# Optimization experiments

Measured on AMD Instinct MI355X. Metric: run time of the kernel, lower is better.

The kernel has to match this reference:

```python
import jax, jax.numpy as jnp
import numpy as np

B, T, D, H = 32, 256, 1024, 1024


def _flip_sequences(x, lengths):
    # Flip only the valid (unpadded) prefix of each sequence, as in flax sst2 util.
    max_len = x.shape[1]
    idxs = (jnp.arange(max_len - 1, -1, -1)[None, :] + lengths[:, None]) % max_len
    return x[jnp.arange(x.shape[0])[:, None], idxs]


def _lstm(x, Wi, Wh, b):
    # OptimizedLSTMCell math: z = x@Wi + h@Wh + b; gates (i, f, g, o);
    # c' = sig(f)*c + sig(i)*tanh(g); h' = sig(o)*tanh(c')
    batch = x.shape[0]
    hid = Wh.shape[0]
    xg = jnp.einsum('btd,dk->btk', x, Wi) + b  # precompute input projections [B,T,4H]

    def step(carry, xg_t):
        c, h = carry
        z = xg_t + h @ Wh
        i, f, g, o = jnp.split(z, 4, axis=-1)
        c = jax.nn.sigmoid(f) * c + jax.nn.sigmoid(i) * jnp.tanh(g)
        h = jax.nn.sigmoid(o) * jnp.tanh(c)
        return (c, h), h

    init = (jnp.zeros((batch, hid), x.dtype), jnp.zeros((batch, hid), x.dtype))
    _, hs = jax.lax.scan(step, init, jnp.swapaxes(xg, 0, 1))  # scan over time
    return jnp.swapaxes(hs, 0, 1)  # [B,T,H]


def setup_inputs() -> dict:
    key = jax.random.key(0)
    ks = jax.random.split(key, 7)
    si = 1.0 / np.sqrt(D)
    sh = 1.0 / np.sqrt(H)
    x = jax.random.normal(ks[0], (B, T, D), dtype=jnp.float32)
    mask = jnp.ones((B, T), dtype=jnp.int32)
    Wi_f = jax.random.normal(ks[1], (D, 4 * H), jnp.float32) * si
    Wh_f = jax.random.normal(ks[2], (H, 4 * H), jnp.float32) * sh
    b_f = jnp.zeros((4 * H,), jnp.float32)
    Wi_b = jax.random.normal(ks[3], (D, 4 * H), jnp.float32) * si
    Wh_b = jax.random.normal(ks[4], (H, 4 * H), jnp.float32) * sh
    b_b = jnp.zeros((4 * H,), jnp.float32)
    return {"x": x, "mask": mask, "Wi_f": Wi_f, "Wh_f": Wh_f, "b_f": b_f,
            "Wi_b": Wi_b, "Wh_b": Wh_b, "b_b": b_b}


def reference(x, mask, Wi_f, Wh_f, b_f, Wi_b, Wh_b, b_b):
    lengths = jnp.sum(mask, axis=1)
    fwd = _lstm(x, Wi_f, Wh_f, b_f)
    x_rev = _flip_sequences(x, lengths)
    bwd = _lstm(x_rev, Wi_b, Wh_b, b_b)
    bwd = _flip_sequences(bwd, lengths)
    return jnp.concatenate([fwd, bwd], axis=-1)  # [B,T,2H]
```

## Files before the change

### kernel.cpp

```cpp
#include <hip/hip_runtime.h>
#include <hip/hip_bf16.h>
#include <stdint.h>

typedef __attribute__((ext_vector_type(4))) float f32x4;
typedef __attribute__((ext_vector_type(8))) short short8;
typedef __attribute__((ext_vector_type(4))) short short4v;

#define OFF_XBF  ((size_t)0)
#define OFF_WIT  ((size_t)16777216)
#define OFF_WHT  ((size_t)33554432)
#define OFF_XG   ((size_t)50331648)
#define OFF_H    ((size_t)184549376)
#define OFF_BIAS ((size_t)184811520)
#define OFF_LEN  ((size_t)184844288)
#define OFF_CNT  ((size_t)184844416)

__device__ __forceinline__ short f2bf(float f) {
  union { float f; uint32_t u; } v; v.f = f;
  uint32_t u = v.u;
  uint32_t r = (u + 0x7fffu + ((u >> 16) & 1u)) >> 16;
  return (short)r;
}
__device__ __forceinline__ float bf2f(short s) {
  union { uint32_t u; float f; } v; v.u = ((uint32_t)(uint16_t)s) << 16;
  return v.f;
}
__device__ __forceinline__ float sigf(float z) {
  float e = __builtin_amdgcn_exp2f(z * -1.44269504f);
  return __builtin_amdgcn_rcpf(1.f + e);
}
__device__ __forceinline__ float tanhfast(float z) {
  float e = __builtin_amdgcn_exp2f(z * -2.88539008f);
  return fmaf(__builtin_amdgcn_rcpf(1.f + e), 2.f, -1.f);
}

__global__ void k_len(const int* __restrict__ mask, int* __restrict__ len) {
  int b = threadIdx.x;
  if (b < 32) {
    int s = 0;
    for (int t = 0; t < 256; t++) s += mask[b * 256 + t];
    len[b] = s;
  }
}

__global__ void k_xconv(const float* __restrict__ x, short* __restrict__ xbf) {
  int bid = blockIdx.x;
  int b = bid >> 8, t = bid & 255;
  int d = threadIdx.x * 4;
  const float* sp = x + ((size_t)bid) * 1024 + d;
  float4 v = *(const float4*)sp;
  short4v o;
  o.x = f2bf(v.x); o.y = f2bf(v.y); o.z = f2bf(v.z); o.w = f2bf(v.w);
  *(short4v*)(xbf + ((size_t)(t * 32 + b)) * 1024 + d) = o;
}

__global__ void k_wprep(const float* __restrict__ Wi_f, const float* __restrict__ Wi_b,
                        const float* __restrict__ Wh_f, const float* __restrict__ Wh_b,
                        short* __restrict__ WiT, short* __restrict__ WhT) {
  __shared__ short ldsT[64 * 72];
  int id = blockIdx.x;
  int which = id >> 11, dir = (id >> 10) & 1, tile = id & 1023;
  int kt = (tile >> 6) * 64, c0 = (tile & 63) * 64;
  const float* src = (which == 0) ? (dir == 0 ? Wi_f : Wi_b)
                                  : (dir == 0 ? Wh_f : Wh_b);
  short* dst = (which == 0) ? WiT : WhT;
  int tid = threadIdx.x;
#pragma unroll 4
  for (int i = 0; i < 16; i++) {
    int idx = i * 256 + tid;
    int kk = idx >> 6, cc = idx & 63;
    float v = src[(size_t)(kt + kk) * 4096 + c0 + cc];
    ldsT[cc * 72 + kk] = f2bf(v);
  }
  __syncthreads();
  int rowc = tid >> 2, part = tid & 3;
  int cg = c0 + rowc;
  int gate = cg >> 10, hc = cg & 1023;
  int p = (hc >> 2) * 16 + gate * 4 + (hc & 3);
  int n = dir * 4096 + p;
  short8 v0 = *(short8*)&ldsT[rowc * 72 + part * 16];
  short8 v1 = *(short8*)&ldsT[rowc * 72 + part * 16 + 8];
  *(short8*)(dst + (size_t)n * 1024 + kt + part * 16) = v0;
  *(short8*)(dst + (size_t)n * 1024 + kt + part * 16 + 8) = v1;
}

__global__ void k_bias(const float* __restrict__ bf_, const float* __restrict__ bb_,
                       float* __restrict__ bp) {
  int n = blockIdx.x * 256 + threadIdx.x;
  int dir = n >> 12, p = n & 4095;
  int gate = (p >> 2) & 3, g4 = p >> 4, h4 = p & 3;
  int c = gate * 1024 + g4 * 4 + h4;
  bp[n] = (dir == 0 ? bf_ : bb_)[c];
}

__global__ void k_gemm(const short* __restrict__ Abf,
                       const short* __restrict__ Bbf,
                       const float* __restrict__ bias,
                       short* __restrict__ C) {
  __shared__ char Ash[128 * 144];
  __shared__ char Bsh[128 * 144];
  const int tid = threadIdx.x;
  const int lane = tid & 63, wid = tid >> 6;
  const int wm = wid >> 1, wn = wid & 1;
  const int l15 = lane & 15, lg = lane >> 4;
  const int m0 = blockIdx.y * 128, n0 = blockIdx.x * 128;

  f32x4 acc[4][4];
#pragma unroll
  for (int i = 0; i < 4; i++)
#pragma unroll
    for (int j = 0; j < 4; j++) acc[i][j] = (f32x4){0.f, 0.f, 0.f, 0.f};

  for (int kt = 0; kt < 1024; kt += 64) {
#pragma unroll
    for (int i = 0; i < 4; i++) {
      int chunk = i * 256 + tid;
      int row = chunk >> 3, kc = chunk & 7;
      *(short8*)(Ash + row * 144 + kc * 16) =
          *(const short8*)(Abf + (size_t)(m0 + row) * 1024 + kt + kc * 8);
      *(short8*)(Bsh + row * 144 + kc * 16) =
          *(const short8*)(Bbf + (size_t)(n0 + row) * 1024 + kt + kc * 8);
    }
    __syncthreads();
#pragma unroll
    for (int kk = 0; kk < 2; kk++) {
      short8 af[4], bfv[4];
#pragma unroll
      for (int mt = 0; mt < 4; mt++)
        af[mt] = *(const short8*)(Ash + (wm * 64 + mt * 16 + l15) * 144 + kk * 64 + lg * 16);
#pragma unroll
      for (int ntc = 0; ntc < 4; ntc++)
        bfv[ntc] = *(const short8*)(Bsh + (wn * 64 + ntc * 16 + l15) * 144 + kk * 64 + lg * 16);
#pragma unroll
      for (int mt = 0; mt < 4; mt++)
#pragma unroll
        for (int ntc = 0; ntc < 4; ntc++)
          acc[mt][ntc] = __builtin_amdgcn_mfma_f32_16x16x32_bf16(af[mt], bfv[ntc], acc[mt][ntc], 0, 0, 0);
    }
    __syncthreads();
  }
  float bs[4];
#pragma unroll
  for (int ntc = 0; ntc < 4; ntc++) bs[ntc] = bias[n0 + wn * 64 + ntc * 16 + l15];
#pragma unroll
  for (int mt = 0; mt < 4; mt++) {
    int row = m0 + wm * 64 + mt * 16 + lg * 4;
#pragma unroll
    for (int ntc = 0; ntc < 4; ntc++) {
      int col = n0 + wn * 64 + ntc * 16 + l15;
#pragma unroll
      for (int r = 0; r < 4; r++)
        C[(size_t)(row + r) * 8192 + col] = f2bf(acc[mt][ntc][r] + bs[ntc]);
    }
  }
}

__global__ void __launch_bounds__(512, 1) k_recur(
    const short* __restrict__ XG,
    const short* __restrict__ WhT,
    const int* __restrict__ len,
    short* __restrict__ hbuf,
    float* __restrict__ out,
    unsigned int* __restrict__ flags) {
  __shared__ char Hld[65536];
  const int tid = threadIdx.x;
  const int lane = tid & 63;
  const int wid = tid >> 6;
  const int bidx = blockIdx.x;
  const int dir = bidx >> 6;
  const int nblk = bidx & 63;
  const int mt = wid >> 2, nt = wid & 3;
  const int l15 = lane & 15, lg = lane >> 4;

  const int ncol = dir * 4096 + nblk * 64 + nt * 16 + l15;
  const short* wrow = WhT + (size_t)ncol * 1024;
  short8 bfr[32];
#pragma unroll
  for (int kk = 0; kk < 32; kk++)
    bfr[kk] = *(const short8*)(wrow + kk * 32 + lg * 8);

  float c_reg[4] = {0.f, 0.f, 0.f, 0.f};
  int lenv[4];
#pragma unroll
  for (int r = 0; r < 4; r++) lenv[r] = len[mt * 16 + lg * 4 + r];

  const int c4 = l15;
  const int gate = c4 >> 2;
  const int brow = mt * 16 + l15;
  const int sw = (brow & 7) << 4;
  const int abase = brow * 2048 + (lg << 4);
  const int hcol0 = nblk * 16 + nt * 4;
  unsigned int* dflags = flags + dir * 64;

  float xg_pf[4];
#pragma unroll
  for (int r = 0; r < 4; r++) {
    int b_r = mt * 16 + lg * 4 + r;
    int tt = (dir == 0) ? 0 : ((lenv[r] - 1) & 255);
    xg_pf[r] = bf2f(XG[(size_t)(tt * 32 + b_r) * 8192 + ncol]);
  }

  for (int t = 0; t < 256; t++) {
    const short* hsrc = hbuf + (size_t)(((t & 1) * 2 + dir) * 32768);
    {
      f32x4 sv[8];
#pragma unroll
      for (int i = 0; i < 8; i++) {
        const short* a = hsrc + (i * 512 + tid) * 8;
        asm volatile("global_load_dwordx4 %0, %1, off sc0 sc1"
                     : "=v"(sv[i]) : "v"(a));
      }
      asm volatile("s_waitcnt vmcnt(0)" ::: "memory");
      __builtin_amdgcn_sched_barrier(0);
#pragma unroll
      for (int i = 0; i < 8; i++) {
        int chunk = i * 512 + tid;
        int row = chunk >> 7;
        *(f32x4*)(Hld + ((chunk * 16) ^ ((row & 7) << 4))) = sv[i];
      }
    }
    __syncthreads();

    f32x4 accA = (f32x4){0.f, 0.f, 0.f, 0.f};
    f32x4 accB = (f32x4){0.f, 0.f, 0.f, 0.f};
#pragma unroll
    for (int kk = 0; kk < 16; kk++) {
      short8 afA = *(const short8*)(Hld + ((abase + kk * 64) ^ sw));
      short8 afB = *(const short8*)(Hld + ((abase + (kk + 16) * 64) ^ sw));
      accA = __builtin_amdgcn_mfma_f32_16x16x32_bf16(afA, bfr[kk], accA, 0, 0, 0);
      accB = __builtin_amdgcn_mfma_f32_16x16x32_bf16(afB, bfr[kk + 16], accB, 0, 0, 0);
    }

    f32x4 hsave[4];
#pragma unroll
    for (int r = 0; r < 4; r++) {
      int b_r = mt * 16 + lg * 4 + r;
      float z = accA[r] + accB[r] + xg_pf[r];
      float s = (gate == 2) ? tanhfast(z) : sigf(z);
      float x8 = __shfl_xor(s, 8);
      float pI = s * x8;
      float v = (gate == 0) ? pI : s;
      float x4 = __shfl_xor(v, 4);
      float o4 = __shfl_xor(x8, 4);
      float cn = fmaf(x4, c_reg[r], pI);
      float h = o4 * tanhfast(cn);
      if (c4 < 4) c_reg[r] = cn;
      uint32_t hb = (uint32_t)(uint16_t)f2bf(h);
      uint32_t p0 = hb | (__shfl_xor(hb, 1) << 16);
      uint32_t q  = __shfl_xor(p0, 2);
      if (c4 == 0) {
        unsigned long long p = (unsigned long long)p0 | ((unsigned long long)q << 32);
        unsigned long long* haddr = (unsigned long long*)
          (hbuf + (size_t)((((t + 1) & 1) * 2 + dir) * 32768) + b_r * 1024 + hcol0);
        __hip_atomic_store(haddr, p, __ATOMIC_RELAXED, __HIP_MEMORY_SCOPE_AGENT);
        hsave[r].x = bf2f((short)(p0 & 0xffff));
        hsave[r].y = bf2f((short)(p0 >> 16));
        hsave[r].z = bf2f((short)(q & 0xffff));
        hsave[r].w = bf2f((short)(q >> 16));
      }
    }

    asm volatile("s_waitcnt vmcnt(0)" ::: "memory");
    __syncthreads();
    if (tid == 0) {
      __hip_atomic_store(dflags + nblk, (unsigned int)(t + 1),
                         __ATOMIC_RELAXED, __HIP_MEMORY_SCOPE_AGENT);
    }
    __builtin_amdgcn_sched_barrier(0);

    if (c4 == 0) {
#pragma unroll
      for (int r = 0; r < 4; r++) {
        int b_r = mt * 16 + lg * 4 + r;
        int tt = (dir == 0) ? t : ((lenv[r] - 1 - t) & 255);
        *(f32x4*)(out + ((size_t)b_r * 256 + tt) * 2048 + dir * 1024 + hcol0) = hsave[r];
      }
    }
    int tn = (t < 255) ? t + 1 : 255;
#pragma unroll
    for (int r = 0; r < 4; r++) {
      int b_r = mt * 16 + lg * 4 + r;
      int tt = (dir == 0) ? tn : ((lenv[r] - 1 - tn) & 255);
      xg_pf[r] = bf2f(XG[(size_t)(tt * 32 + b_r) * 8192 + ncol]);
    }

    if (wid == 0) {
      const unsigned int* fl = dflags + lane;
      unsigned int tgt = (unsigned int)(t + 1);
      for (;;) {
        unsigned int v = __hip_atomic_load(fl, __ATOMIC_RELAXED, __HIP_MEMORY_SCOPE_AGENT);
        if (__all((int)(v >= tgt))) break;
      }
    }
    __builtin_amdgcn_sched_barrier(0);
    __syncthreads();
  }
}

extern "C" void kernel_launch(void* const* d_in, const int* in_sizes, int n_in,
                              void* d_out, int out_size, void* d_ws, size_t ws_size,
                              hipStream_t stream) {
  const float* x    = (const float*)d_in[0];
  const int*   mask = (const int*)d_in[1];
  const float* Wi_f = (const float*)d_in[2];
  const float* Wh_f = (const float*)d_in[3];
  const float* b_f  = (const float*)d_in[4];
  const float* Wi_b = (const float*)d_in[5];
  const float* Wh_b = (const float*)d_in[6];
  const float* b_b  = (const float*)d_in[7];
  float* out = (float*)d_out;
  char* ws = (char*)d_ws;

  short* xbf  = (short*)(ws + OFF_XBF);
  short* WiT  = (short*)(ws + OFF_WIT);
  short* WhT  = (short*)(ws + OFF_WHT);
  short* XG   = (short*)(ws + OFF_XG);
  short* hbuf = (short*)(ws + OFF_H);
  float* bp   = (float*)(ws + OFF_BIAS);
  int*   len  = (int*)(ws + OFF_LEN);
  unsigned int* flags = (unsigned int*)(ws + OFF_CNT);

  hipMemsetAsync(hbuf, 0, 262144, stream);
  hipMemsetAsync(flags, 0, 512, stream);

  k_len<<<1, 64, 0, stream>>>(mask, len);
  k_xconv<<<8192, 256, 0, stream>>>(x, xbf);
  k_wprep<<<4096, 256, 0, stream>>>(Wi_f, Wi_b, Wh_f, Wh_b, WiT, WhT);
  k_bias<<<32, 256, 0, stream>>>(b_f, b_b, bp);

  dim3 g(64, 64);
  k_gemm<<<g, 256, 0, stream>>>(xbf, WiT, bp, XG);

  k_recur<<<128, 512, 0, stream>>>(XG, WhT, len, hbuf, out, flags);
}
```

Before: 1.481 ms.

## Stage h in LDS per block and wait per-producer flags before loading slices

Each block now collects its h slice in a small LDS buffer and publishes it with one contiguous 16-byte store per lane from wave 0, instead of scattered 8-byte atomic stores. The hbuf layout becomes block-major, so each block's slice is contiguous. The end-of-step global barrier is removed. Each wave instead spins only on the 8 producer flags whose slices it loads, then loads them right away, which lets waves start as soon as their inputs are ready. In exchange the layout and swizzle math change, and correctness depends on the flag/store ordering with relaxed atomics and sc0 sc1 stores.

```diff
diff --git a/kernel.cpp b/kernel.cpp
--- a/kernel.cpp
+++ b/kernel.cpp
@@ -162,7 +162,9 @@
     short* __restrict__ hbuf,
     float* __restrict__ out,
     unsigned int* __restrict__ flags) {
-  __shared__ char Hld[65536];
+  __shared__ char Hld[66560];
+  char* Pub = Hld + 65536;
+  char* hb = (char*)hbuf;
   const int tid = threadIdx.x;
   const int lane = tid & 63;
   const int wid = tid >> 6;
@@ -200,23 +202,32 @@
     xg_pf[r] = bf2f(XG[(size_t)(tt * 32 + b_r) * 8192 + ncol]);
   }
 
+  const int myb = lane >> 1;
+  const int mysw = (myb & 7) << 4;
+  const int mybase = myb * 2048 + (lane & 1) * 16;
+
   for (int t = 0; t < 256; t++) {
-    const short* hsrc = hbuf + (size_t)(((t & 1) * 2 + dir) * 32768);
     {
+      const unsigned int* fl = dflags + wid * 8 + (lane & 7);
+      unsigned int tgt = (unsigned int)t;
+      for (;;) {
+        unsigned int v = __hip_atomic_load(fl, __ATOMIC_RELAXED, __HIP_MEMORY_SCOPE_AGENT);
+        if (__all((int)(v >= tgt))) break;
+      }
+      __builtin_amdgcn_sched_barrier(0);
+      const char* hsrcB = hb + (size_t)(((t & 1) * 2 + dir) * 65536);
       f32x4 sv[8];
 #pragma unroll
-      for (int i = 0; i < 8; i++) {
-        const short* a = hsrc + (i * 512 + tid) * 8;
-        asm volatile("global_load_dwordx4 %0, %1, off sc0 sc1"
-                     : "=v"(sv[i]) : "v"(a));
+      for (int j = 0; j < 8; j++) {
+        const char* a = hsrcB + (wid * 8 + j) * 1024 + lane * 16;
+        asm volatile("global_load_dwordx4 %0, %1, off sc0 sc1" : "=v"(sv[j]) : "v"(a));
       }
       asm volatile("s_waitcnt vmcnt(0)" ::: "memory");
       __builtin_amdgcn_sched_barrier(0);
 #pragma unroll
-      for (int i = 0; i < 8; i++) {
-        int chunk = i * 512 + tid;
-        int row = chunk >> 7;
-        *(f32x4*)(Hld + ((chunk * 16) ^ ((row & 7) << 4))) = sv[i];
+      for (int j = 0; j < 8; j++) {
+        int off = (mybase + (wid * 8 + j) * 32) ^ mysw;
+        *(f32x4*)(Hld + off) = sv[j];
       }
     }
     __syncthreads();
@@ -245,26 +256,28 @@
       float cn = fmaf(x4, c_reg[r], pI);
       float h = o4 * tanhfast(cn);
       if (c4 < 4) c_reg[r] = cn;
-      uint32_t hb = (uint32_t)(uint16_t)f2bf(h);
-      uint32_t p0 = hb | (__shfl_xor(hb, 1) << 16);
+      uint32_t hb16 = (uint32_t)(uint16_t)f2bf(h);
+      uint32_t p0 = hb16 | (__shfl_xor(hb16, 1) << 16);
       uint32_t q  = __shfl_xor(p0, 2);
       if (c4 == 0) {
         unsigned long long p = (unsigned long long)p0 | ((unsigned long long)q << 32);
-        unsigned long long* haddr = (unsigned long long*)
-          (hbuf + (size_t)((((t + 1) & 1) * 2 + dir) * 32768) + b_r * 1024 + hcol0);
-        __hip_atomic_store(haddr, p, __ATOMIC_RELAXED, __HIP_MEMORY_SCOPE_AGENT);
+        *(unsigned long long*)(Pub + b_r * 32 + nt * 8) = p;
         hsave[r].x = bf2f((short)(p0 & 0xffff));
         hsave[r].y = bf2f((short)(p0 >> 16));
         hsave[r].z = bf2f((short)(q & 0xffff));
         hsave[r].w = bf2f((short)(q >> 16));
       }
     }
-
-    asm volatile("s_waitcnt vmcnt(0)" ::: "memory");
     __syncthreads();
-    if (tid == 0) {
-      __hip_atomic_store(dflags + nblk, (unsigned int)(t + 1),
-                         __ATOMIC_RELAXED, __HIP_MEMORY_SCOPE_AGENT);
+
+    if (wid == 0) {
+      f32x4 pv = *(const f32x4*)(Pub + lane * 16);
+      char* hdstB = hb + (size_t)((((t + 1) & 1) * 2 + dir) * 65536) + nblk * 1024 + lane * 16;
+      asm volatile("global_store_dwordx4 %0, %1, off sc0 sc1" :: "v"(hdstB), "v"(pv) : "memory");
+      asm volatile("s_waitcnt vmcnt(0)" ::: "memory");
+      if (lane == 0)
+        __hip_atomic_store(dflags + nblk, (unsigned int)(t + 1),
+                           __ATOMIC_RELAXED, __HIP_MEMORY_SCOPE_AGENT);
     }
     __builtin_amdgcn_sched_barrier(0);
 
@@ -283,17 +296,6 @@
       int tt = (dir == 0) ? tn : ((lenv[r] - 1 - tn) & 255);
       xg_pf[r] = bf2f(XG[(size_t)(tt * 32 + b_r) * 8192 + ncol]);
     }
-
-    if (wid == 0) {
-      const unsigned int* fl = dflags + lane;
-      unsigned int tgt = (unsigned int)(t + 1);
-      for (;;) {
-        unsigned int v = __hip_atomic_load(fl, __ATOMIC_RELAXED, __HIP_MEMORY_SCOPE_AGENT);
-        if (__all((int)(v >= tgt))) break;
-      }
-    }
-    __builtin_amdgcn_sched_barrier(0);
-    __syncthreads();
   }
 }
 
```

Result: faster. 1.365 ms (-7.8%).
